# Optimization experiments

Hardware: AMD Instinct MI355X
Metric: run time of the kernel (lower is better)

The kernel has to match this reference:

```python
import jax, jax.numpy as jnp
import numpy as np

B, S, HID, H = 4, 1024, 1024, 16
D = HID // H


def setup_inputs() -> dict:
    key = jax.random.key(0)
    ks = jax.random.split(key, 4)
    scale = 0.02
    return {
        "hidden_states": jax.random.normal(ks[0], (B, S, HID), dtype=jnp.float32),
        "attention_mask": jnp.ones((B, S), dtype=jnp.int32),
        "layer_head_mask": jnp.ones((H,), dtype=jnp.float32),
        "Wq": jax.random.normal(ks[1], (HID, HID), dtype=jnp.float32) * scale,
        "bq": jnp.zeros((HID,), dtype=jnp.float32),
        "Wk": jax.random.normal(ks[2], (HID, HID), dtype=jnp.float32) * scale,
        "bk": jnp.zeros((HID,), dtype=jnp.float32),
        "Wv": jax.random.normal(ks[3], (HID, HID), dtype=jnp.float32) * scale,
        "bv": jnp.zeros((HID,), dtype=jnp.float32),
    }


def reference(hidden_states, attention_mask, layer_head_mask, Wq, bq, Wk, bk, Wv, bv):
    b, s, _ = hidden_states.shape
    # QKV projections, split heads: [B,S,H,D]
    q = (hidden_states @ Wq + bq).reshape(b, s, H, D)
    k = (hidden_states @ Wk + bk).reshape(b, s, H, D)
    v = (hidden_states @ Wv + bv).reshape(b, s, H, D)

    # attention bias from padding mask: [B,1,1,S]
    mask = attention_mask[:, None, None, :]
    neg = jnp.finfo(jnp.float32).min
    bias = jnp.where(mask > 0, 0.0, neg).astype(jnp.float32)

    # dot_product_attention_weights: scale query by 1/sqrt(D)
    q = q / jnp.sqrt(jnp.asarray(D, dtype=q.dtype))
    scores = jnp.einsum("bqhd,bkhd->bhqk", q, k) + bias  # [B,H,S,S]
    attn_weights = jax.nn.softmax(scores, axis=-1)

    # per-head masking
    attn_weights = attn_weights * layer_head_mask[None, :, None, None]

    attn_output = jnp.einsum("bhqk,bkhd->bqhd", attn_weights, v)
    return attn_output.reshape(b, s, HID)
```

## Files before the change

kernel.cpp:

```cpp
#include <hip/hip_runtime.h>
#include <stdint.h>

typedef __bf16 bf16_t;
typedef bf16_t __attribute__((ext_vector_type(8))) bf16x8;
typedef float __attribute__((ext_vector_type(4))) f32x4;
typedef float __attribute__((ext_vector_type(16))) f32x16;
typedef unsigned u32;

#define BATCH 4
#define SEQ 1024
#define HIDD 1024
#define NH 16
#define DH 64

__device__ __forceinline__ unsigned short f2bf(float f) {
  unsigned u = __float_as_uint(f);
  u += 0x7fffu + ((u >> 16) & 1u);
  return (unsigned short)(u >> 16);
}

__device__ __forceinline__ f32x4 mfma16(bf16x8 a, bf16x8 b, f32x4 c) {
  return __builtin_amdgcn_mfma_f32_16x16x32_bf16(a, b, c, 0, 0, 0);
}
__device__ __forceinline__ f32x16 mfma32(bf16x8 a, bf16x8 b, f32x16 c) {
  return __builtin_amdgcn_mfma_f32_32x32x16_bf16(a, b, c, 0, 0, 0);
}

__device__ __forceinline__ void gload_lds16(const void* g, void* l) {
  __builtin_amdgcn_global_load_lds(
      (__attribute__((address_space(1))) void*)(uintptr_t)g,
      (__attribute__((address_space(3))) void*)l, 16, 0, 0);
}

__device__ __forceinline__ u32 cvtpk(float lo, float hi) {
  u32 r;
  asm("v_cvt_pk_bf16_f32 %0, %1, %2" : "=v"(r) : "v"(lo), "v"(hi));
  return r;
}
__device__ __forceinline__ void plswap(u32& a, u32& b) {
  asm("v_permlane32_swap_b32 %0, %1" : "+v"(a), "+v"(b));
}

__global__ void hs2bf(const float* __restrict__ x, unsigned short* __restrict__ y) {
  const int i = blockIdx.x * 256 + threadIdx.x;
  const float4 f = ((const float4*)x)[i];
  ushort4 o = make_ushort4(f2bf(f.x), f2bf(f.y), f2bf(f.z), f2bf(f.w));
  ((ushort4*)y)[i] = o;
}

__global__ __launch_bounds__(256) void wtrans(
    const float* __restrict__ Wq, const float* __restrict__ Wk,
    const float* __restrict__ Wv, unsigned short* __restrict__ Wt) {
  __shared__ unsigned short tile[64][72];
  const int z = blockIdx.z;
  const float* W = (z == 0) ? Wq : (z == 1) ? Wk : Wv;
  unsigned short* o = Wt + (size_t)z * (1024 * 1024);
  const int k0 = blockIdx.x * 64, n0 = blockIdx.y * 64;
  const int r = threadIdx.x >> 6, c = threadIdx.x & 63;
#pragma unroll
  for (int i = 0; i < 16; ++i) {
    const int row = i * 4 + r;
    tile[row][c] = f2bf(W[(size_t)(k0 + row) * 1024 + n0 + c]);
  }
  __syncthreads();
#pragma unroll
  for (int i = 0; i < 16; ++i) {
    const int row = i * 4 + r;
    o[(size_t)(n0 + row) * 1024 + k0 + c] = tile[c][row];
  }
}

__global__ __launch_bounds__(256) void qkv_gemm(
    const unsigned short* __restrict__ A,
    const unsigned short* __restrict__ Wt,
    const float* __restrict__ bq, const float* __restrict__ bk,
    const float* __restrict__ bv,
    unsigned short* __restrict__ outb) {
  __shared__ alignas(16) unsigned short Alds[128 * 32];
  __shared__ alignas(16) unsigned short Blds[128 * 32];

  const int z = blockIdx.z;
  const unsigned short* Bt = Wt + (size_t)z * (1024 * 1024);
  const float* bias = (z == 0) ? bq : (z == 1) ? bk : bv;
  unsigned short* outp = outb + (size_t)z * (4096 * 1024);
  const float scale = (z == 0) ? 0.125f * 1.44269504089f : 1.0f;

  const int m0 = blockIdx.x * 128;
  const int n0 = blockIdx.y * 128;
  const int t = threadIdx.x;
  const int w = t >> 6, l = t & 63;
  const int lg = l >> 4, lc = l & 15;
  const int wr = w >> 1, wc = w & 1;

  f32x4 acc[4][4] = {};

  for (int kt = 0; kt < 1024; kt += 32) {
    __syncthreads();
#pragma unroll
    for (int i = 0; i < 2; ++i) {
      const int c = i * 256 + t;
      const int row = c >> 2;
      const int kp = (c & 3) * 8;
      gload_lds16(A + (size_t)(m0 + row) * 1024 + kt + kp,
                  (char*)Alds + i * 4096 + w * 1024);
      gload_lds16(Bt + (size_t)(n0 + row) * 1024 + kt + kp,
                  (char*)Blds + i * 4096 + w * 1024);
    }
    __syncthreads();

    bf16x8 af[4], bfr[4];
#pragma unroll
    for (int m = 0; m < 4; ++m)
      af[m] = *(const bf16x8*)(Alds + (wr * 64 + m * 16 + lc) * 32 + lg * 8);
#pragma unroll
    for (int n = 0; n < 4; ++n)
      bfr[n] = *(const bf16x8*)(Blds + (wc * 64 + n * 16 + lc) * 32 + lg * 8);
#pragma unroll
    for (int m = 0; m < 4; ++m)
#pragma unroll
      for (int n = 0; n < 4; ++n)
        acc[m][n] = mfma16(af[m], bfr[n], acc[m][n]);
  }

#pragma unroll
  for (int n = 0; n < 4; ++n) {
    const int col = n0 + wc * 64 + n * 16 + lc;
    const float bs = bias[col];
#pragma unroll
    for (int m = 0; m < 4; ++m)
#pragma unroll
      for (int r = 0; r < 4; ++r) {
        const int row = m0 + wr * 64 + m * 16 + lg * 4 + r;
        outp[(size_t)row * 1024 + col] = f2bf((acc[m][n][r] + bs) * scale);
      }
  }
}

__global__ __launch_bounds__(256) void kpack_kernel(
    const unsigned short* __restrict__ K, unsigned short* __restrict__ Kp) {
  const int kb = blockIdx.x, bh = blockIdx.y;
  const int b = bh >> 4, h = bh & 15;
  const int t = threadIdx.x, l = t & 63, s = t >> 6;
  const unsigned short* src = K + (size_t)(b * 1024 + kb * 32 + (l & 31)) * 1024 +
                              h * 64 + s * 16 + ((l >> 5) & 1) * 8;
  const uint4 v = *(const uint4*)src;
  *(uint4*)(Kp + ((size_t)(bh * 32 + kb) * 4 + s) * 512 + l * 8) = v;
}

__global__ __launch_bounds__(256) void vpack_kernel(
    const unsigned short* __restrict__ V, unsigned short* __restrict__ Vp) {
  __shared__ unsigned short tile[64][72];
  const int tt = blockIdx.x;
  const int hh = blockIdx.y;
  const int t = threadIdx.x;
#pragma unroll
  for (int i = 0; i < 2; ++i) {
    const int c = i * 256 + t;
    const int row = c >> 3, cp = c & 7;
    *(uint4*)&tile[row][cp * 8] =
        *(const uint4*)(V + (size_t)(tt * 64 + row) * 1024 + hh * 64 + cp * 8);
  }
  __syncthreads();
  const int b = tt >> 4, kt = tt & 15;
  const int bh = b * 16 + hh;
#pragma unroll
  for (int i = 0; i < 2; ++i) {
    const int c = i * 256 + t;
    const int l = c & 63, s = (c >> 6) & 3, g = c >> 8;
    const int kl = s * 16 + ((l >> 5) & 1) * 8;
    const int d = g * 32 + (l & 31);
    unsigned short buf[8];
#pragma unroll
    for (int e = 0; e < 8; ++e) buf[e] = tile[kl + e][d];
    *(uint4*)(Vp + ((size_t)(bh * 16 + kt) * 8 + g * 4 + s) * 512 + l * 8) =
        *(uint4*)buf;
  }
}

__global__ __launch_bounds__(256, 2) void attn_kernel(
    const unsigned short* __restrict__ Qb,
    const unsigned short* __restrict__ Kpack,
    const unsigned short* __restrict__ Vpack,
    const int* __restrict__ amask,
    const float* __restrict__ lhm,
    float* __restrict__ out) {
  const int id = blockIdx.x;
  const int swzid = (id & 7) * 64 + (id >> 3);
  const int qt = swzid & 7;
  const int bh = swzid >> 3;
  const int b = bh >> 4, h = bh & 15;
  const int t = threadIdx.x;
  const int w = t >> 6, l = t & 63;
  const int lo = l & 31, hi = l >> 5;
  const int q0 = qt * 128 + w * 32;

  const unsigned short* Kp = Kpack + (size_t)bh * 65536 + l * 8;
  const unsigned short* Vp = Vpack + (size_t)bh * 65536 + l * 8;

  const unsigned short* qp = Qb + (size_t)(b * SEQ + q0 + lo) * HIDD + h * DH + hi * 8;
  bf16x8 qf[4];
#pragma unroll
  for (int s = 0; s < 4; ++s) qf[s] = *(const bf16x8*)(qp + s * 16);

  bool needmask;
  {
    unsigned long long mm = ~0ull;
#pragma unroll
    for (int tk = 0; tk < 16; ++tk)
      mm &= __ballot(amask[b * SEQ + tk * 64 + l] > 0);
    needmask = (mm != ~0ull);
  }

  float m_run = -INFINITY, l_run = 0.f;
  f32x16 acc0 = {}, acc1 = {};

  bf16x8 kf0[4], kf1[4], vf0[4], vf1[4];

#pragma unroll
  for (int s = 0; s < 4; ++s) {
    kf0[s] = *(const bf16x8*)(Kp + (s)*512);
    kf1[s] = *(const bf16x8*)(Kp + (4 + s) * 512);
  }

  for (int tk = 0; tk < 16; ++tk) {
#pragma unroll
    for (int s = 0; s < 4; ++s) {
      vf0[s] = *(const bf16x8*)(Vp + (size_t)(tk * 8 + s) * 512);
      vf1[s] = *(const bf16x8*)(Vp + (size_t)(tk * 8 + 4 + s) * 512);
    }

    f32x16 sg0 = {}, sg1 = {};
    __builtin_amdgcn_s_setprio(1);
#pragma unroll
    for (int s = 0; s < 4; ++s) {
      sg0 = mfma32(kf0[s], qf[s], sg0);
      sg1 = mfma32(kf1[s], qf[s], sg1);
    }
    __builtin_amdgcn_s_setprio(0);

    if (tk < 15) {
#pragma unroll
      for (int s = 0; s < 4; ++s) {
        kf0[s] = *(const bf16x8*)(Kp + (size_t)(tk * 8 + 8 + s) * 512);
        kf1[s] = *(const bf16x8*)(Kp + (size_t)(tk * 8 + 12 + s) * 512);
      }
    }

    float t0[8];
#pragma unroll
    for (int i = 0; i < 8; ++i)
      t0[i] = fmaxf(fmaxf(sg0[i], sg0[i + 8]), fmaxf(sg1[i], sg1[i + 8]));
    float t1 = fmaxf(fmaxf(fmaxf(t0[0], t0[1]), fmaxf(t0[2], t0[3])),
                     fmaxf(fmaxf(t0[4], t0[5]), fmaxf(t0[6], t0[7])));
    const float pmax = fmaxf(t1, __shfl_xor(t1, 32));

    if (!__all(pmax <= m_run + 8.f)) {
      const float mnew = fmaxf(m_run, pmax);
      const float sc = __builtin_amdgcn_exp2f(m_run - mnew);
      m_run = mnew;
      l_run *= sc;
#pragma unroll
      for (int g = 0; g < 16; ++g) {
        const int rowi = (g & 3) + 8 * (g >> 2) + 4 * hi;
        const float scr = __shfl(sc, rowi);
        acc0[g] *= scr;
        acc1[g] *= scr;
      }
    }

#pragma unroll
    for (int g = 0; g < 16; ++g) {
      sg0[g] = __builtin_amdgcn_exp2f(sg0[g] - m_run);
      sg1[g] = __builtin_amdgcn_exp2f(sg1[g] - m_run);
    }

    if (needmask) {
      const int mv = amask[b * SEQ + tk * 64 + l];
      const unsigned long long m64 = __ballot(mv > 0);
      if (m64 != ~0ull) {
#pragma unroll
        for (int g = 0; g < 16; ++g) {
          const int krow = (g & 3) + 8 * (g >> 2) + 4 * hi;
          if (!((m64 >> krow) & 1)) sg0[g] = 0.f;
          if (!((m64 >> (krow + 32)) & 1)) sg1[g] = 0.f;
        }
      }
    }

    float s0[8];
#pragma unroll
    for (int i = 0; i < 8; ++i)
      s0[i] = (sg0[i] + sg0[i + 8]) + (sg1[i] + sg1[i + 8]);
    float rs = ((s0[0] + s0[1]) + (s0[2] + s0[3])) +
               ((s0[4] + s0[5]) + (s0[6] + s0[7]));
    rs += __shfl_xor(rs, 32);
    l_run += rs;

    auto mk = [](float a0, float a1, float a2, float a3,
                 float a4, float a5, float a6, float a7) -> bf16x8 {
      u32 x = cvtpk(a0, a1), y = cvtpk(a2, a3);
      u32 a = cvtpk(a4, a5), b2 = cvtpk(a6, a7);
      plswap(x, a);
      plswap(y, b2);
      union { u32 u[4]; bf16x8 v; } fu;
      fu.u[0] = x; fu.u[1] = y; fu.u[2] = a; fu.u[3] = b2;
      return fu.v;
    };
    const bf16x8 pa0 = mk(sg0[0], sg0[1], sg0[2], sg0[3], sg0[4], sg0[5], sg0[6], sg0[7]);
    const bf16x8 pa1 = mk(sg0[8], sg0[9], sg0[10], sg0[11], sg0[12], sg0[13], sg0[14], sg0[15]);
    const bf16x8 pa2 = mk(sg1[0], sg1[1], sg1[2], sg1[3], sg1[4], sg1[5], sg1[6], sg1[7]);
    const bf16x8 pa3 = mk(sg1[8], sg1[9], sg1[10], sg1[11], sg1[12], sg1[13], sg1[14], sg1[15]);

    __builtin_amdgcn_s_setprio(1);
#pragma unroll
    for (int s = 0; s < 4; ++s) {
      const bf16x8 paf = (s == 0) ? pa0 : (s == 1) ? pa1 : (s == 2) ? pa2 : pa3;
      acc0 = mfma32(paf, vf0[s], acc0);
      acc1 = mfma32(paf, vf1[s], acc1);
    }
    __builtin_amdgcn_s_setprio(0);
  }

  const float hm = lhm[h];
  const float inv = hm / l_run;
  float* ob = out + (size_t)(b * SEQ + q0) * HIDD + h * DH + lo;
#pragma unroll
  for (int g = 0; g < 16; ++g) {
    const int rowi = (g & 3) + 8 * (g >> 2) + 4 * hi;
    const float iv = __shfl(inv, rowi);
    ob[(size_t)rowi * HIDD] = acc0[g] * iv;
    ob[(size_t)rowi * HIDD + 32] = acc1[g] * iv;
  }
}

extern "C" void kernel_launch(void* const* d_in, const int* in_sizes, int n_in,
                              void* d_out, int out_size, void* d_ws, size_t ws_size,
                              hipStream_t stream) {
  const float* hs = (const float*)d_in[0];
  const int* amask = (const int*)d_in[1];
  const float* lhm = (const float*)d_in[2];
  const float* Wq = (const float*)d_in[3];
  const float* bq = (const float*)d_in[4];
  const float* Wk = (const float*)d_in[5];
  const float* bk = (const float*)d_in[6];
  const float* Wv = (const float*)d_in[7];
  const float* bv = (const float*)d_in[8];
  float* out = (float*)d_out;

  char* ws = (char*)d_ws;
  unsigned short* HSbf = (unsigned short*)ws;
  unsigned short* Wt = (unsigned short*)(ws + (8u << 20));
  unsigned short* QKV = (unsigned short*)(ws + (14u << 20));
  unsigned short* Kpk = (unsigned short*)ws;
  unsigned short* Vpk = (unsigned short*)(ws + (38u << 20));

  hs2bf<<<4096, 256, 0, stream>>>(hs, HSbf);
  wtrans<<<dim3(16, 16, 3), 256, 0, stream>>>(Wq, Wk, Wv, Wt);
  qkv_gemm<<<dim3(32, 8, 3), 256, 0, stream>>>(HSbf, Wt, bq, bk, bv, QKV);
  kpack_kernel<<<dim3(32, 64), 256, 0, stream>>>(QKV + (size_t)4096 * 1024, Kpk);
  vpack_kernel<<<dim3(64, 16), 256, 0, stream>>>(QKV + (size_t)2 * 4096 * 1024, Vpk);
  attn_kernel<<<512, 256, 0, stream>>>(QKV, Kpk, Vpk, amask, lhm, out);
}
```

Baseline: 85.96 us.

## Stage K/V tiles through double-buffered LDS via direct global-to-LDS loads

```diff
diff --git a/kernel.cpp b/kernel.cpp
--- a/kernel.cpp
+++ b/kernel.cpp
@@ -184,6 +184,9 @@
     const int* __restrict__ amask,
     const float* __restrict__ lhm,
     float* __restrict__ out) {
+  __shared__ alignas(16) char K_lds[2][8192];
+  __shared__ alignas(16) char V_lds[2][8192];
+
   const int id = blockIdx.x;
   const int swzid = (id & 7) * 64 + (id >> 3);
   const int qt = swzid & 7;
@@ -194,8 +197,9 @@
   const int lo = l & 31, hi = l >> 5;
   const int q0 = qt * 128 + w * 32;
 
-  const unsigned short* Kp = Kpack + (size_t)bh * 65536 + l * 8;
-  const unsigned short* Vp = Vpack + (size_t)bh * 65536 + l * 8;
+  const unsigned short* KpT = Kpack + (size_t)bh * 65536;
+  const unsigned short* VpT = Vpack + (size_t)bh * 65536;
+  const int soff = w * 512 + l * 8;
 
   const unsigned short* qp = Qb + (size_t)(b * SEQ + q0 + lo) * HIDD + h * DH + hi * 8;
   bf16x8 qf[4];
@@ -204,29 +208,49 @@
 
   bool needmask;
   {
-    unsigned long long mm = ~0ull;
-#pragma unroll
-    for (int tk = 0; tk < 16; ++tk)
-      mm &= __ballot(amask[b * SEQ + tk * 64 + l] > 0);
-    needmask = (mm != ~0ull);
+    int andv = 1;
+#pragma unroll
+    for (int tkk = 0; tkk < 16; ++tkk)
+      andv &= (amask[b * SEQ + tkk * 64 + l] > 0) ? 1 : 0;
+    needmask = (__ballot(andv != 0) != ~0ull);
   }
 
   float m_run = -INFINITY, l_run = 0.f;
   f32x16 acc0 = {}, acc1 = {};
 
-  bf16x8 kf0[4], kf1[4], vf0[4], vf1[4];
-
-#pragma unroll
-  for (int s = 0; s < 4; ++s) {
-    kf0[s] = *(const bf16x8*)(Kp + (s)*512);
-    kf1[s] = *(const bf16x8*)(Kp + (4 + s) * 512);
-  }
+  auto stage = [&](int tk, int buf) {
+    const unsigned short* ks = KpT + tk * 4096 + soff;
+    const unsigned short* vs = VpT + tk * 4096 + soff;
+    gload_lds16(ks, &K_lds[buf][w * 1024]);
+    gload_lds16(ks + 2048, &K_lds[buf][4096 + w * 1024]);
+    gload_lds16(vs, &V_lds[buf][w * 1024]);
+    gload_lds16(vs + 2048, &V_lds[buf][4096 + w * 1024]);
+  };
+
+  stage(0, 0);
 
   for (int tk = 0; tk < 16; ++tk) {
+    const int cur = tk & 1;
+
+    if (tk < 15) {
+      stage(tk + 1, cur ^ 1);
+      asm volatile("s_waitcnt vmcnt(4)" ::: "memory");
+    } else {
+      asm volatile("s_waitcnt vmcnt(0)" ::: "memory");
+    }
+    __builtin_amdgcn_s_barrier();
+    __builtin_amdgcn_sched_barrier(0);
+
+    const char* kb = K_lds[cur];
+    const char* vb = V_lds[cur];
+
+    bf16x8 kf0[4], kf1[4], vf0[4], vf1[4];
 #pragma unroll
     for (int s = 0; s < 4; ++s) {
-      vf0[s] = *(const bf16x8*)(Vp + (size_t)(tk * 8 + s) * 512);
-      vf1[s] = *(const bf16x8*)(Vp + (size_t)(tk * 8 + 4 + s) * 512);
+      kf0[s] = *(const bf16x8*)(kb + s * 1024 + l * 16);
+      kf1[s] = *(const bf16x8*)(kb + 4096 + s * 1024 + l * 16);
+      vf0[s] = *(const bf16x8*)(vb + s * 1024 + l * 16);
+      vf1[s] = *(const bf16x8*)(vb + 4096 + s * 1024 + l * 16);
     }
 
     f32x16 sg0 = {}, sg1 = {};
@@ -237,14 +261,6 @@
       sg1 = mfma32(kf1[s], qf[s], sg1);
     }
     __builtin_amdgcn_s_setprio(0);
-
-    if (tk < 15) {
-#pragma unroll
-      for (int s = 0; s < 4; ++s) {
-        kf0[s] = *(const bf16x8*)(Kp + (size_t)(tk * 8 + 8 + s) * 512);
-        kf1[s] = *(const bf16x8*)(Kp + (size_t)(tk * 8 + 12 + s) * 512);
-      }
-    }
 
     float t0[8];
 #pragma unroll
@@ -319,6 +335,8 @@
       acc1 = mfma32(paf, vf1[s], acc1);
     }
     __builtin_amdgcn_s_setprio(0);
+
+    __builtin_amdgcn_s_barrier();
   }
 
   const float hm = lhm[h];
```

New measurement: 87.36 us. Within noise of the previous version (+1.6%).
